# Kernel optimization log

Hardware: AMD Instinct MI355X
Metric: run time of the kernel (lower is better)

Reference implementation:

```python
import jax, jax.numpy as jnp
import numpy as np

N_LAGS = 64
EPS = 1e-8


def setup_inputs() -> dict:
    key = jax.random.key(0)
    x = jax.random.normal(key, (16, 8, 250, 1024), dtype=jnp.float32)
    return {"x": x}


def reference(x):
    B, M, T, L = x.shape
    # rfft over all mics once (shared across pairs)
    X = jnp.fft.rfft(x, axis=-1)  # [B, M, T, L//2+1] complex
    # all mic pairs (m1 < m2), row-major order matching the torch double loop
    i1, i2 = np.triu_indices(M, k=1)
    X1 = X[:, i1]  # [B, P, T, F]
    X2 = X[:, i2]  # [B, P, T, F]
    R = X1 * jnp.conj(X2)
    R = R / (jnp.abs(R) + EPS)  # PHAT weighting
    cc = jnp.fft.irfft(R, n=L, axis=-1)        # [B, P, T, L]
    cc = jnp.fft.fftshift(cc, axes=-1)
    center = L // 2
    start = center - N_LAGS // 2
    return cc[..., start:start + N_LAGS]        # [B, P, T, n_lags]
```

## Files before the change

kernel.cpp:

```cpp
#include <hip/hip_runtime.h>
#include <math.h>

#define B_    16
#define M_    8
#define T_    250
#define L_    1024
#define NPAIR 28

#define KTOT   1024
#define CH_K   128
#define NKT    4
#define NCHUNK 8

typedef _Float16 half8  __attribute__((ext_vector_type(8)));
typedef _Float16 half2t __attribute__((ext_vector_type(2)));
typedef float    floatx4 __attribute__((ext_vector_type(4)));

__device__ __align__(16) _Float16 g_Btw[64 * KTOT];

__constant__ int c_i1[NPAIR] = {0,0,0,0,0,0,0,1,1,1,1,1,1,2,2,2,2,2,3,3,3,3,4,4,4,5,5,6};
__constant__ int c_i2[NPAIR] = {1,2,3,4,5,6,7,2,3,4,5,6,7,3,4,5,6,7,4,5,6,7,5,6,7,6,7,7};

__global__ void init_btw() {
    int idx = blockIdx.x * 256 + threadIdx.x;
    int n = idx >> 10, k = idx & 1023;
    float v;
    if (k == 0)      v = 1.0f / 1024.0f;
    else if (k == 1) v = (n & 1) ? (-1.0f / 1024.0f) : (1.0f / 1024.0f);
    else {
        int bin = k >> 1, tau = n - 32;
        int r = (tau * bin) & 1023;
        float ang = (float)r * (6.283185307179586f / 1024.0f);
        float s, c; sincosf(ang, &s, &c);
        v = ((k & 1) ? -s : c) * (2.0f / 1024.0f);
    }
    g_Btw[idx] = (_Float16)v;
}

#define PHI(i) ((i) ^ (((i) >> 4) & 15) ^ ((((i) >> 8) & 3) << 1))
#define AXR(p) (8 * ((p) & 7))

__device__ inline float2 cmul(float2 a, float2 b) {
    return make_float2(fmaf(a.x, b.x, -a.y * b.y), fmaf(a.x, b.y, a.y * b.x));
}
__device__ inline float2 cadd(float2 a, float2 b) { return make_float2(a.x + b.x, a.y + b.y); }
__device__ inline float2 csub(float2 a, float2 b) { return make_float2(a.x - b.x, a.y - b.y); }
__device__ inline float2 cmni(float2 a) { return make_float2(a.y, -a.x); }

__device__ inline void dft8(float2 v[8]) {
    const float rt = 0.70710678118654752440f;
    float2 b0 = cadd(v[0], v[4]), b1 = cadd(v[1], v[5]);
    float2 b2 = cadd(v[2], v[6]), b3 = cadd(v[3], v[7]);
    float2 c0 = csub(v[0], v[4]);
    float2 t1 = csub(v[1], v[5]);
    float2 c1 = make_float2(rt * (t1.x + t1.y), rt * (t1.y - t1.x));
    float2 c2 = cmni(csub(v[2], v[6]));
    float2 t3 = csub(v[3], v[7]);
    float2 c3 = make_float2(rt * (t3.y - t3.x), -rt * (t3.x + t3.y));
    float2 f0 = cadd(b0, b2), f1 = cadd(b1, b3);
    float2 g0 = csub(b0, b2), g1 = cmni(csub(b1, b3));
    v[0] = cadd(f0, f1); v[4] = csub(f0, f1);
    v[2] = cadd(g0, g1); v[6] = csub(g0, g1);
    f0 = cadd(c0, c2); f1 = cadd(c1, c3);
    g0 = csub(c0, c2); g1 = cmni(csub(c1, c3));
    v[1] = cadd(f0, f1); v[5] = csub(f0, f1);
    v[3] = cadd(g0, g1); v[7] = csub(g0, g1);
}

__device__ inline void twiddle8(float2 v[8], float2 w1) {
    float2 w = w1;
    v[1] = cmul(v[1], w);
#pragma unroll
    for (int k = 2; k < 8; ++k) { w = cmul(w, w1); v[k] = cmul(v[k], w); }
}

__device__ inline int posmap(int k) {
    return ((k & 1) << 9) | (((k >> 1) & 7) << 6) | (((k >> 4) & 7) << 3) | ((k >> 7) & 7);
}

__global__ __launch_bounds__(512, 8) void gcc_main(const float* __restrict__ x,
                                                   float* __restrict__ out) {
    __shared__ float2 s_z[4 * 1024];
    __shared__ __align__(16) _Float16 sA[32 * CH_K];

    const int tid = threadIdx.x;
    const int t = blockIdx.x, b = blockIdx.y;
    const int f = tid & 127, c = tid >> 7;
    float2* Zb = s_z + c * 1024;

    float ws, wc;
    sincosf((float)f * (-6.283185307179586f / 1024.0f), &ws, &wc);
    const float2 w = make_float2(wc, ws);

    {
        const float* xa = x + (((size_t)b * M_ + 2 * c) * T_ + t) * L_;
        const float* xb = xa + (size_t)T_ * L_;
        float va[8], vb[8];
#pragma unroll
        for (int j = 0; j < 8; ++j) { va[j] = xa[f + 128 * j]; vb[j] = xb[f + 128 * j]; }
        const float rt = 0.70710678118654752440f;
#pragma unroll
        for (int q = 0; q < 4; ++q) {
            float2 a = make_float2(va[q], vb[q]);
            float2 d = make_float2(va[q + 4], vb[q + 4]);
            float2 tq = cmul(csub(a, d), w);
            float2 r;
            if (q == 0)      r = tq;
            else if (q == 1) r = make_float2(rt * (tq.x + tq.y), rt * (tq.y - tq.x));
            else if (q == 2) r = make_float2(tq.y, -tq.x);
            else             r = make_float2(rt * (tq.y - tq.x), -rt * (tq.x + tq.y));
            Zb[PHI(f + 128 * q)]       = cadd(a, d);
            Zb[PHI(f + 128 * q + 512)] = r;
        }
    }
    __syncthreads();

    {
        float2 wl = w;
        if (f & 64) wl = cmul(wl, make_float2(0.92387953251128674f, 0.38268343236508977f));
        const float2 wB = cmul(wl, wl);
        const int base = (f >> 6) * 512 + (f & 63);
        float2 v[8];
#pragma unroll
        for (int r = 0; r < 8; ++r) v[r] = Zb[PHI(base + 64 * r)];
        dft8(v);
        twiddle8(v, wB);
#pragma unroll
        for (int k = 0; k < 8; ++k) Zb[PHI(base + 64 * k)] = v[k];
    }
    __syncthreads();

    {
        float s2, c2;
        sincosf((float)(f & 7) * (-6.283185307179586f / 64.0f), &s2, &c2);
        const float2 wC = make_float2(c2, s2);
        const int base = (f >> 3) * 64 + (f & 7);
        float2 v[8];
#pragma unroll
        for (int r = 0; r < 8; ++r) v[r] = Zb[PHI(base + 8 * r)];
        dft8(v);
        twiddle8(v, wC);
#pragma unroll
        for (int k = 0; k < 8; ++k) Zb[PHI(base + 8 * k)] = v[k];
    }
    __syncthreads();

    {
        const int base = f * 8;
        float2 v[8];
#pragma unroll
        for (int r = 0; r < 8; ++r) v[r] = Zb[PHI(base + r)];
        dft8(v);
#pragma unroll
        for (int k = 0; k < 8; ++k) Zb[PHI(base + k)] = v[k];
    }
    __syncthreads();

    const int lane = tid & 63, wv = tid >> 6;
    const int mt = wv >> 2, nt = wv & 3;
    const int l15 = lane & 15, quad = lane >> 4;
    const int arow = mt * 16 + l15;
    const _Float16* Bbase = g_Btw + (nt * 16 + l15) * KTOT;
    floatx4 acc = {0.0f, 0.0f, 0.0f, 0.0f};

    const int bl = lane;
    const int pg = wv;

    if (tid < 256) ((unsigned int*)sA)[1792 + tid] = 0u;

#define PAIRA(p_, a_, b_)                                                     \
    {                                                                         \
        float2 X1 = Xs[a_], X2 = Xs[b_];                                      \
        float rr = X1.x * X2.x + X1.y * X2.y;                                 \
        float ri = X1.y * X2.x - X1.x * X2.y;                                 \
        float m2 = rr * rr + ri * ri;                                         \
        float inv = (m2 > 1e-30f) ? rsqrtf(m2) : 0.0f;                        \
        *(half2t*)&sA[(p_) * CH_K + ((2 * bl) ^ AXR(p_))] =                   \
            (half2t){(_Float16)(rr * inv), (_Float16)(ri * inv)};             \
    }

    auto fillA = [&](int h) {
        const int beta = h * 64 + bl;
        const int pa = posmap(beta);
        const int pb = posmap((1024 - beta) & 1023);
        float2 Xs[8];
#pragma unroll
        for (int cc = 0; cc < 4; ++cc) {
            float2 Aa = s_z[cc * 1024 + PHI(pa)];
            float2 Bb = s_z[cc * 1024 + PHI(pb)];
            Xs[2 * cc]     = make_float2(0.5f * (Aa.x + Bb.x), 0.5f * (Aa.y - Bb.y));
            Xs[2 * cc + 1] = make_float2(0.5f * (Aa.y + Bb.y), 0.5f * (Bb.x - Aa.x));
        }
        if (pg == 0) {
            PAIRA(0, 0, 1) PAIRA(1, 0, 2) PAIRA(2, 0, 3) PAIRA(3, 0, 4)
        } else if (pg == 1) {
            PAIRA(4, 0, 5) PAIRA(5, 0, 6) PAIRA(6, 0, 7) PAIRA(7, 1, 2)
        } else if (pg == 2) {
            PAIRA(8, 1, 3) PAIRA(9, 1, 4) PAIRA(10, 1, 5) PAIRA(11, 1, 6)
        } else if (pg == 3) {
            PAIRA(12, 1, 7) PAIRA(13, 2, 3) PAIRA(14, 2, 4) PAIRA(15, 2, 5)
        } else if (pg == 4) {
            PAIRA(16, 2, 6) PAIRA(17, 2, 7) PAIRA(18, 3, 4)
        } else if (pg == 5) {
            PAIRA(19, 3, 5) PAIRA(20, 3, 6) PAIRA(21, 3, 7)
        } else if (pg == 6) {
            PAIRA(22, 4, 5) PAIRA(23, 4, 6) PAIRA(24, 4, 7)
        } else {
            PAIRA(25, 5, 6) PAIRA(26, 5, 7) PAIRA(27, 6, 7)
        }
        if (h == 0 && bl == 0) {
            const int p0 = (pg < 4) ? 4 * pg : 16 + 3 * (pg - 4);
            const int cnt = (pg < 4) ? 4 : 3;
            const int pN = 4;
#pragma unroll
            for (int pp = 0; pp < cnt; ++pp) {
                const int p = p0 + pp;
                float2 Za = s_z[(c_i1[p] >> 1) * 1024 + pN];
                float2 Zc = s_z[(c_i2[p] >> 1) * 1024 + pN];
                float x1 = (c_i1[p] & 1) ? Za.y : Za.x;
                float x2 = (c_i2[p] & 1) ? Zc.y : Zc.x;
                float rr = x1 * x2;
                float inv = (rr * rr > 1e-30f) ? rsqrtf(rr * rr) : 0.0f;
                sA[p * CH_K + (1 ^ AXR(p))] = (_Float16)(rr * inv);
            }
        }
    };

    for (int h = 0; h < NCHUNK; ++h) {
        fillA(h);
        __syncthreads();

        const _Float16* Bp = Bbase + h * CH_K;
        const int ax = AXR(arow);
#pragma unroll
        for (int kt = 0; kt < NKT; ++kt) {
            half8 af = *(const half8*)(sA + arow * CH_K + ((kt * 32 + quad * 8) ^ ax));
            half8 bf = *(const half8*)(Bp + kt * 32 + quad * 8);
            acc = __builtin_amdgcn_mfma_f32_16x16x32_f16(af, bf, acc, 0, 0, 0);
        }
        __syncthreads();
    }

#pragma unroll
    for (int r = 0; r < 4; ++r) {
        int pair = mt * 16 + quad * 4 + r;
        if (pair < NPAIR)
            out[((((size_t)b * NPAIR + pair) * T_ + t) << 6) + nt * 16 + l15] = acc[r];
    }
}

extern "C" void kernel_launch(void* const* d_in, const int* in_sizes, int n_in,
                              void* d_out, int out_size, void* d_ws, size_t ws_size,
                              hipStream_t stream) {
    (void)in_sizes; (void)n_in; (void)d_ws; (void)ws_size; (void)out_size;
    hipLaunchKernelGGL(init_btw, dim3(256), dim3(256), 0, stream);
    hipLaunchKernelGGL(gcc_main, dim3(T_, B_), dim3(512), 0, stream,
                       (const float*)d_in[0], (float*)d_out);
}
```

Baseline: 320.6 us.

## Split fused FFT+PHAT+DFT kernel into FFT kernel and separate MFMA matmul kernel

The single fused kernel is split in two. The first does the per-frame FFT and PHAT weighting and writes the normalized cross-spectra as fp16 to a large global buffer. The second is a dedicated MFMA kernel where each wave computes all 28 pairs by 64 lags for one frame over the full K=1024, with more accumulators per wave. This removes per-chunk shared-memory staging and barriers from the matmul, but adds a write and read of a roughly 229 MB intermediate and one more kernel launch.

```diff
diff --git a/kernel.cpp b/kernel.cpp
--- a/kernel.cpp
+++ b/kernel.cpp
@@ -6,17 +6,14 @@
 #define T_    250
 #define L_    1024
 #define NPAIR 28
-
-#define KTOT   1024
-#define CH_K   128
-#define NKT    4
-#define NCHUNK 8
+#define NBT   (B_ * T_)
 
 typedef _Float16 half8  __attribute__((ext_vector_type(8)));
 typedef _Float16 half2t __attribute__((ext_vector_type(2)));
 typedef float    floatx4 __attribute__((ext_vector_type(4)));
 
-__device__ __align__(16) _Float16 g_Btw[64 * KTOT];
+__device__ __align__(16) _Float16 g_Btw[64 * 1024];
+__device__ __align__(16) _Float16 g_A[((size_t)NBT * NPAIR + 64) * 1024];
 
 __constant__ int c_i1[NPAIR] = {0,0,0,0,0,0,0,1,1,1,1,1,1,2,2,2,2,2,3,3,3,3,4,4,4,5,5,6};
 __constant__ int c_i2[NPAIR] = {1,2,3,4,5,6,7,2,3,4,5,6,7,3,4,5,6,7,4,5,6,7,5,6,7,6,7,7};
@@ -38,7 +35,6 @@
 }
 
 #define PHI(i) ((i) ^ (((i) >> 4) & 15) ^ ((((i) >> 8) & 3) << 1))
-#define AXR(p) (8 * ((p) & 7))
 
 __device__ inline float2 cmul(float2 a, float2 b) {
     return make_float2(fmaf(a.x, b.x, -a.y * b.y), fmaf(a.x, b.y, a.y * b.x));
@@ -78,10 +74,8 @@
     return ((k & 1) << 9) | (((k >> 1) & 7) << 6) | (((k >> 4) & 7) << 3) | ((k >> 7) & 7);
 }
 
-__global__ __launch_bounds__(512, 8) void gcc_main(const float* __restrict__ x,
-                                                   float* __restrict__ out) {
+__global__ __launch_bounds__(512, 6) void gcc_fft(const float* __restrict__ x) {
     __shared__ float2 s_z[4 * 1024];
-    __shared__ __align__(16) _Float16 sA[32 * CH_K];
 
     const int tid = threadIdx.x;
     const int t = blockIdx.x, b = blockIdx.y;
@@ -156,31 +150,23 @@
     }
     __syncthreads();
 
-    const int lane = tid & 63, wv = tid >> 6;
-    const int mt = wv >> 2, nt = wv & 3;
-    const int l15 = lane & 15, quad = lane >> 4;
-    const int arow = mt * 16 + l15;
-    const _Float16* Bbase = g_Btw + (nt * 16 + l15) * KTOT;
-    floatx4 acc = {0.0f, 0.0f, 0.0f, 0.0f};
-
-    const int bl = lane;
-    const int pg = wv;
-
-    if (tid < 256) ((unsigned int*)sA)[1792 + tid] = 0u;
-
-#define PAIRA(p_, a_, b_)                                                     \
+    const int bl = tid & 127, pg = tid >> 7;
+    const size_t abase = ((size_t)b * T_ + t) * (size_t)(NPAIR * 1024);
+
+#define PAIRG(p_, a_, b_)                                                     \
     {                                                                         \
         float2 X1 = Xs[a_], X2 = Xs[b_];                                      \
         float rr = X1.x * X2.x + X1.y * X2.y;                                 \
         float ri = X1.y * X2.x - X1.x * X2.y;                                 \
         float m2 = rr * rr + ri * ri;                                         \
         float inv = (m2 > 1e-30f) ? rsqrtf(m2) : 0.0f;                        \
-        *(half2t*)&sA[(p_) * CH_K + ((2 * bl) ^ AXR(p_))] =                   \
+        *(half2t*)&g_A[abase + (p_) * 1024 + 2 * beta] =                      \
             (half2t){(_Float16)(rr * inv), (_Float16)(ri * inv)};             \
     }
 
-    auto fillA = [&](int h) {
-        const int beta = h * 64 + bl;
+#pragma unroll 1
+    for (int h = 0; h < 4; ++h) {
+        const int beta = h * 128 + bl;
         const int pa = posmap(beta);
         const int pb = posmap((1024 - beta) & 1023);
         float2 Xs[8];
@@ -192,60 +178,81 @@
             Xs[2 * cc + 1] = make_float2(0.5f * (Aa.y + Bb.y), 0.5f * (Bb.x - Aa.x));
         }
         if (pg == 0) {
-            PAIRA(0, 0, 1) PAIRA(1, 0, 2) PAIRA(2, 0, 3) PAIRA(3, 0, 4)
+            PAIRG(0, 0, 1) PAIRG(1, 0, 2) PAIRG(2, 0, 3) PAIRG(3, 0, 4)
+            PAIRG(4, 0, 5) PAIRG(5, 0, 6) PAIRG(6, 0, 7)
         } else if (pg == 1) {
-            PAIRA(4, 0, 5) PAIRA(5, 0, 6) PAIRA(6, 0, 7) PAIRA(7, 1, 2)
+            PAIRG(7, 1, 2) PAIRG(8, 1, 3) PAIRG(9, 1, 4) PAIRG(10, 1, 5)
+            PAIRG(11, 1, 6) PAIRG(12, 1, 7) PAIRG(13, 2, 3)
         } else if (pg == 2) {
-            PAIRA(8, 1, 3) PAIRA(9, 1, 4) PAIRA(10, 1, 5) PAIRA(11, 1, 6)
-        } else if (pg == 3) {
-            PAIRA(12, 1, 7) PAIRA(13, 2, 3) PAIRA(14, 2, 4) PAIRA(15, 2, 5)
-        } else if (pg == 4) {
-            PAIRA(16, 2, 6) PAIRA(17, 2, 7) PAIRA(18, 3, 4)
-        } else if (pg == 5) {
-            PAIRA(19, 3, 5) PAIRA(20, 3, 6) PAIRA(21, 3, 7)
-        } else if (pg == 6) {
-            PAIRA(22, 4, 5) PAIRA(23, 4, 6) PAIRA(24, 4, 7)
+            PAIRG(14, 2, 4) PAIRG(15, 2, 5) PAIRG(16, 2, 6) PAIRG(17, 2, 7)
+            PAIRG(18, 3, 4) PAIRG(19, 3, 5) PAIRG(20, 3, 6)
         } else {
-            PAIRA(25, 5, 6) PAIRA(26, 5, 7) PAIRA(27, 6, 7)
+            PAIRG(21, 3, 7) PAIRG(22, 4, 5) PAIRG(23, 4, 6) PAIRG(24, 4, 7)
+            PAIRG(25, 5, 6) PAIRG(26, 5, 7) PAIRG(27, 6, 7)
         }
         if (h == 0 && bl == 0) {
-            const int p0 = (pg < 4) ? 4 * pg : 16 + 3 * (pg - 4);
-            const int cnt = (pg < 4) ? 4 : 3;
             const int pN = 4;
 #pragma unroll
-            for (int pp = 0; pp < cnt; ++pp) {
-                const int p = p0 + pp;
+            for (int pp = 0; pp < 7; ++pp) {
+                const int p = pg * 7 + pp;
                 float2 Za = s_z[(c_i1[p] >> 1) * 1024 + pN];
                 float2 Zc = s_z[(c_i2[p] >> 1) * 1024 + pN];
                 float x1 = (c_i1[p] & 1) ? Za.y : Za.x;
                 float x2 = (c_i2[p] & 1) ? Zc.y : Zc.x;
                 float rr = x1 * x2;
                 float inv = (rr * rr > 1e-30f) ? rsqrtf(rr * rr) : 0.0f;
-                sA[p * CH_K + (1 ^ AXR(p))] = (_Float16)(rr * inv);
+                g_A[abase + p * 1024 + 1] = (_Float16)(rr * inv);
             }
         }
-    };
-
-    for (int h = 0; h < NCHUNK; ++h) {
-        fillA(h);
-        __syncthreads();
-
-        const _Float16* Bp = Bbase + h * CH_K;
-        const int ax = AXR(arow);
-#pragma unroll
-        for (int kt = 0; kt < NKT; ++kt) {
-            half8 af = *(const half8*)(sA + arow * CH_K + ((kt * 32 + quad * 8) ^ ax));
-            half8 bf = *(const half8*)(Bp + kt * 32 + quad * 8);
-            acc = __builtin_amdgcn_mfma_f32_16x16x32_f16(af, bf, acc, 0, 0, 0);
-        }
-        __syncthreads();
-    }
-
+    }
+}
+
+__global__ __launch_bounds__(256, 4) void gcc_mm(float* __restrict__ out) {
+    const int lane = threadIdx.x & 63, wv = threadIdx.x >> 6;
+    const int bt = blockIdx.x * 4 + wv;
+    const int l15 = lane & 15, quad = lane >> 4;
+    const int b = bt / T_, t = bt - b * T_;
+
+    const _Float16* Ap0 = g_A + ((size_t)bt * NPAIR + l15) * 1024 + quad * 8;
+    const _Float16* Ap1 = Ap0 + 16 * 1024;
+    const _Float16* Bp  = g_Btw + (size_t)l15 * 1024 + quad * 8;
+
+    floatx4 acc00 = {0,0,0,0}, acc01 = {0,0,0,0}, acc02 = {0,0,0,0}, acc03 = {0,0,0,0};
+    floatx4 acc10 = {0,0,0,0}, acc11 = {0,0,0,0}, acc12 = {0,0,0,0}, acc13 = {0,0,0,0};
+
+#pragma unroll 4
+    for (int kt = 0; kt < 32; ++kt) {
+        half8 a0 = *(const half8*)(Ap0 + kt * 32);
+        half8 a1 = *(const half8*)(Ap1 + kt * 32);
+        half8 b0 = *(const half8*)(Bp + 0 * 16384 + kt * 32);
+        half8 b1 = *(const half8*)(Bp + 1 * 16384 + kt * 32);
+        half8 b2 = *(const half8*)(Bp + 2 * 16384 + kt * 32);
+        half8 b3 = *(const half8*)(Bp + 3 * 16384 + kt * 32);
+        acc00 = __builtin_amdgcn_mfma_f32_16x16x32_f16(a0, b0, acc00, 0, 0, 0);
+        acc10 = __builtin_amdgcn_mfma_f32_16x16x32_f16(a1, b0, acc10, 0, 0, 0);
+        acc01 = __builtin_amdgcn_mfma_f32_16x16x32_f16(a0, b1, acc01, 0, 0, 0);
+        acc11 = __builtin_amdgcn_mfma_f32_16x16x32_f16(a1, b1, acc11, 0, 0, 0);
+        acc02 = __builtin_amdgcn_mfma_f32_16x16x32_f16(a0, b2, acc02, 0, 0, 0);
+        acc12 = __builtin_amdgcn_mfma_f32_16x16x32_f16(a1, b2, acc12, 0, 0, 0);
+        acc03 = __builtin_amdgcn_mfma_f32_16x16x32_f16(a0, b3, acc03, 0, 0, 0);
+        acc13 = __builtin_amdgcn_mfma_f32_16x16x32_f16(a1, b3, acc13, 0, 0, 0);
+    }
+
+    const size_t obase = (((size_t)b * NPAIR) * T_ + t) << 6;
 #pragma unroll
     for (int r = 0; r < 4; ++r) {
-        int pair = mt * 16 + quad * 4 + r;
-        if (pair < NPAIR)
-            out[((((size_t)b * NPAIR + pair) * T_ + t) << 6) + nt * 16 + l15] = acc[r];
+        int p0 = quad * 4 + r;
+        out[obase + ((size_t)p0 * T_ << 6) + 0 * 16 + l15] = acc00[r];
+        out[obase + ((size_t)p0 * T_ << 6) + 1 * 16 + l15] = acc01[r];
+        out[obase + ((size_t)p0 * T_ << 6) + 2 * 16 + l15] = acc02[r];
+        out[obase + ((size_t)p0 * T_ << 6) + 3 * 16 + l15] = acc03[r];
+        int p1 = 16 + quad * 4 + r;
+        if (p1 < NPAIR) {
+            out[obase + ((size_t)p1 * T_ << 6) + 0 * 16 + l15] = acc10[r];
+            out[obase + ((size_t)p1 * T_ << 6) + 1 * 16 + l15] = acc11[r];
+            out[obase + ((size_t)p1 * T_ << 6) + 2 * 16 + l15] = acc12[r];
+            out[obase + ((size_t)p1 * T_ << 6) + 3 * 16 + l15] = acc13[r];
+        }
     }
 }
 
@@ -254,6 +261,6 @@
                               hipStream_t stream) {
     (void)in_sizes; (void)n_in; (void)d_ws; (void)ws_size; (void)out_size;
     hipLaunchKernelGGL(init_btw, dim3(256), dim3(256), 0, stream);
-    hipLaunchKernelGGL(gcc_main, dim3(T_, B_), dim3(512), 0, stream,
-                       (const float*)d_in[0], (float*)d_out);
-}
+    hipLaunchKernelGGL(gcc_fft, dim3(T_, B_), dim3(512), 0, stream, (const float*)d_in[0]);
+    hipLaunchKernelGGL(gcc_mm, dim3(NBT / 4), dim3(256), 0, stream, (float*)d_out);
+}
```

Measured after the change: 362.3 us. +13.0%, slower.

## Double-buffer PHAT A tiles and prefetch twiddle B fragments into registers

Applied to the files above, without the earlier changes.

The A operand in shared memory is now double-buffered, so the next chunk's PHAT-normalised cross-spectrum is written while MFMAs consume the current one. This removes one barrier per chunk. The twiddle-matrix B fragments for the next chunk are loaded into registers one iteration ahead. The XOR swizzle is replaced by a padded row pitch of 136, and the launch-bounds occupancy hint drops from 8 to 4. The cost is more LDS per block and more registers, which may lower occupancy. Rows 28-31 of the A buffers are no longer zeroed, which relies on those MFMA output rows never being written.

```diff
diff --git a/kernel.cpp b/kernel.cpp
--- a/kernel.cpp
+++ b/kernel.cpp
@@ -7,16 +7,17 @@
 #define L_    1024
 #define NPAIR 28
 
-#define KTOT   1024
 #define CH_K   128
 #define NKT    4
 #define NCHUNK 8
+#define APITCH 136
+#define ABUF   (32 * APITCH)
 
 typedef _Float16 half8  __attribute__((ext_vector_type(8)));
 typedef _Float16 half2t __attribute__((ext_vector_type(2)));
 typedef float    floatx4 __attribute__((ext_vector_type(4)));
 
-__device__ __align__(16) _Float16 g_Btw[64 * KTOT];
+__device__ __align__(16) _Float16 g_Btw[64 * 1024];
 
 __constant__ int c_i1[NPAIR] = {0,0,0,0,0,0,0,1,1,1,1,1,1,2,2,2,2,2,3,3,3,3,4,4,4,5,5,6};
 __constant__ int c_i2[NPAIR] = {1,2,3,4,5,6,7,2,3,4,5,6,7,3,4,5,6,7,4,5,6,7,5,6,7,6,7,7};
@@ -38,7 +39,6 @@
 }
 
 #define PHI(i) ((i) ^ (((i) >> 4) & 15) ^ ((((i) >> 8) & 3) << 1))
-#define AXR(p) (8 * ((p) & 7))
 
 __device__ inline float2 cmul(float2 a, float2 b) {
     return make_float2(fmaf(a.x, b.x, -a.y * b.y), fmaf(a.x, b.y, a.y * b.x));
@@ -78,10 +78,10 @@
     return ((k & 1) << 9) | (((k >> 1) & 7) << 6) | (((k >> 4) & 7) << 3) | ((k >> 7) & 7);
 }
 
-__global__ __launch_bounds__(512, 8) void gcc_main(const float* __restrict__ x,
+__global__ __launch_bounds__(512, 4) void gcc_main(const float* __restrict__ x,
                                                    float* __restrict__ out) {
     __shared__ float2 s_z[4 * 1024];
-    __shared__ __align__(16) _Float16 sA[32 * CH_K];
+    __shared__ __align__(16) _Float16 sA[2 * ABUF];
 
     const int tid = threadIdx.x;
     const int t = blockIdx.x, b = blockIdx.y;
@@ -160,13 +160,11 @@
     const int mt = wv >> 2, nt = wv & 3;
     const int l15 = lane & 15, quad = lane >> 4;
     const int arow = mt * 16 + l15;
-    const _Float16* Bbase = g_Btw + (nt * 16 + l15) * KTOT;
+    const _Float16* Bbase = g_Btw + (size_t)(nt * 16 + l15) * 1024 + quad * 8;
     floatx4 acc = {0.0f, 0.0f, 0.0f, 0.0f};
 
     const int bl = lane;
     const int pg = wv;
-
-    if (tid < 256) ((unsigned int*)sA)[1792 + tid] = 0u;
 
 #define PAIRA(p_, a_, b_)                                                     \
     {                                                                         \
@@ -175,11 +173,11 @@
         float ri = X1.y * X2.x - X1.x * X2.y;                                 \
         float m2 = rr * rr + ri * ri;                                         \
         float inv = (m2 > 1e-30f) ? rsqrtf(m2) : 0.0f;                        \
-        *(half2t*)&sA[(p_) * CH_K + ((2 * bl) ^ AXR(p_))] =                   \
+        *(half2t*)&dst[(p_) * APITCH + 2 * bl] =                              \
             (half2t){(_Float16)(rr * inv), (_Float16)(ri * inv)};             \
     }
 
-    auto fillA = [&](int h) {
+    auto fillA = [&](int h, _Float16* dst) {
         const int beta = h * 64 + bl;
         const int pa = posmap(beta);
         const int pb = posmap((1024 - beta) & 1023);
@@ -221,24 +219,35 @@
                 float x2 = (c_i2[p] & 1) ? Zc.y : Zc.x;
                 float rr = x1 * x2;
                 float inv = (rr * rr > 1e-30f) ? rsqrtf(rr * rr) : 0.0f;
-                sA[p * CH_K + (1 ^ AXR(p))] = (_Float16)(rr * inv);
+                dst[p * APITCH + 1] = (_Float16)(rr * inv);
             }
         }
     };
 
+    half8 bc[4], bn[4];
+#pragma unroll
+    for (int kt = 0; kt < NKT; ++kt) bc[kt] = *(const half8*)(Bbase + kt * 32);
+
+    fillA(0, sA);
+    __syncthreads();
+
+#pragma unroll
     for (int h = 0; h < NCHUNK; ++h) {
-        fillA(h);
-        __syncthreads();
-
-        const _Float16* Bp = Bbase + h * CH_K;
-        const int ax = AXR(arow);
+        if (h < NCHUNK - 1) {
+            const _Float16* Bn = Bbase + (h + 1) * CH_K;
+#pragma unroll
+            for (int kt = 0; kt < NKT; ++kt) bn[kt] = *(const half8*)(Bn + kt * 32);
+            fillA(h + 1, sA + ((h + 1) & 1) * ABUF);
+        }
+        const _Float16* Ap = sA + (h & 1) * ABUF + arow * APITCH;
 #pragma unroll
         for (int kt = 0; kt < NKT; ++kt) {
-            half8 af = *(const half8*)(sA + arow * CH_K + ((kt * 32 + quad * 8) ^ ax));
-            half8 bf = *(const half8*)(Bp + kt * 32 + quad * 8);
-            acc = __builtin_amdgcn_mfma_f32_16x16x32_f16(af, bf, acc, 0, 0, 0);
-        }
-        __syncthreads();
+            half8 af = *(const half8*)(Ap + kt * 32 + quad * 8);
+            acc = __builtin_amdgcn_mfma_f32_16x16x32_f16(af, bc[kt], acc, 0, 0, 0);
+        }
+#pragma unroll
+        for (int kt = 0; kt < NKT; ++kt) bc[kt] = bn[kt];
+        if (h < NCHUNK - 1) __syncthreads();
     }
 
 #pragma unroll
```

Result: slower. 373.2 us (+16.4%).

## Double GEMM K-chunk, use padded sA pitch, and rebalance pair-fill work

Applied to the files above, without the earlier changes.

The PHAT-weighted A tile now covers 256 frequency columns instead of 128. That halves the fill/MFMA rounds and the block-wide barriers. The XOR swizzle on sA is replaced by a padded row pitch of 264. Pair normalization is redistributed so each 128-thread group handles 7 pairs. The twiddle powers are computed as a shallower tree rather than a serial chain, and launch bounds drop to 4 blocks/SM to match the larger LDS footprint. The zero-fill of the unused A rows is removed; those rows only feed outputs that are never written.

```diff
diff --git a/kernel.cpp b/kernel.cpp
--- a/kernel.cpp
+++ b/kernel.cpp
@@ -8,9 +8,10 @@
 #define NPAIR 28
 
 #define KTOT   1024
-#define CH_K   128
-#define NKT    4
-#define NCHUNK 8
+#define CH_K   256
+#define NKT    8
+#define NCHUNK 4
+#define APITCH 264
 
 typedef _Float16 half8  __attribute__((ext_vector_type(8)));
 typedef _Float16 half2t __attribute__((ext_vector_type(2)));
@@ -38,7 +39,6 @@
 }
 
 #define PHI(i) ((i) ^ (((i) >> 4) & 15) ^ ((((i) >> 8) & 3) << 1))
-#define AXR(p) (8 * ((p) & 7))
 
 __device__ inline float2 cmul(float2 a, float2 b) {
     return make_float2(fmaf(a.x, b.x, -a.y * b.y), fmaf(a.x, b.y, a.y * b.x));
@@ -68,20 +68,25 @@
 }
 
 __device__ inline void twiddle8(float2 v[8], float2 w1) {
-    float2 w = w1;
-    v[1] = cmul(v[1], w);
-#pragma unroll
-    for (int k = 2; k < 8; ++k) { w = cmul(w, w1); v[k] = cmul(v[k], w); }
+    float2 w2 = cmul(w1, w1);
+    float2 w3 = cmul(w2, w1);
+    float2 w4 = cmul(w2, w2);
+    float2 w5 = cmul(w4, w1);
+    float2 w6 = cmul(w4, w2);
+    float2 w7 = cmul(w4, w3);
+    v[1] = cmul(v[1], w1); v[2] = cmul(v[2], w2); v[3] = cmul(v[3], w3);
+    v[4] = cmul(v[4], w4); v[5] = cmul(v[5], w5); v[6] = cmul(v[6], w6);
+    v[7] = cmul(v[7], w7);
 }
 
 __device__ inline int posmap(int k) {
     return ((k & 1) << 9) | (((k >> 1) & 7) << 6) | (((k >> 4) & 7) << 3) | ((k >> 7) & 7);
 }
 
-__global__ __launch_bounds__(512, 8) void gcc_main(const float* __restrict__ x,
+__global__ __launch_bounds__(512, 4) void gcc_main(const float* __restrict__ x,
                                                    float* __restrict__ out) {
     __shared__ float2 s_z[4 * 1024];
-    __shared__ __align__(16) _Float16 sA[32 * CH_K];
+    __shared__ __align__(16) _Float16 sA[32 * APITCH];
 
     const int tid = threadIdx.x;
     const int t = blockIdx.x, b = blockIdx.y;
@@ -163,10 +168,7 @@
     const _Float16* Bbase = g_Btw + (nt * 16 + l15) * KTOT;
     floatx4 acc = {0.0f, 0.0f, 0.0f, 0.0f};
 
-    const int bl = lane;
-    const int pg = wv;
-
-    if (tid < 256) ((unsigned int*)sA)[1792 + tid] = 0u;
+    const int bl = tid & 127, pg = tid >> 7;
 
 #define PAIRA(p_, a_, b_)                                                     \
     {                                                                         \
@@ -175,12 +177,12 @@
         float ri = X1.y * X2.x - X1.x * X2.y;                                 \
         float m2 = rr * rr + ri * ri;                                         \
         float inv = (m2 > 1e-30f) ? rsqrtf(m2) : 0.0f;                        \
-        *(half2t*)&sA[(p_) * CH_K + ((2 * bl) ^ AXR(p_))] =                   \
+        *(half2t*)&sA[(p_) * APITCH + 2 * bl] =                               \
             (half2t){(_Float16)(rr * inv), (_Float16)(ri * inv)};             \
     }
 
     auto fillA = [&](int h) {
-        const int beta = h * 64 + bl;
+        const int beta = h * 128 + bl;
         const int pa = posmap(beta);
         const int pb = posmap((1024 - beta) & 1023);
         float2 Xs[8];
@@ -193,35 +195,29 @@
         }
         if (pg == 0) {
             PAIRA(0, 0, 1) PAIRA(1, 0, 2) PAIRA(2, 0, 3) PAIRA(3, 0, 4)
+            PAIRA(4, 0, 5) PAIRA(5, 0, 6) PAIRA(6, 0, 7)
         } else if (pg == 1) {
-            PAIRA(4, 0, 5) PAIRA(5, 0, 6) PAIRA(6, 0, 7) PAIRA(7, 1, 2)
+            PAIRA(7, 1, 2) PAIRA(8, 1, 3) PAIRA(9, 1, 4) PAIRA(10, 1, 5)
+            PAIRA(11, 1, 6) PAIRA(12, 1, 7) PAIRA(13, 2, 3)
         } else if (pg == 2) {
-            PAIRA(8, 1, 3) PAIRA(9, 1, 4) PAIRA(10, 1, 5) PAIRA(11, 1, 6)
-        } else if (pg == 3) {
-            PAIRA(12, 1, 7) PAIRA(13, 2, 3) PAIRA(14, 2, 4) PAIRA(15, 2, 5)
-        } else if (pg == 4) {
-            PAIRA(16, 2, 6) PAIRA(17, 2, 7) PAIRA(18, 3, 4)
-        } else if (pg == 5) {
-            PAIRA(19, 3, 5) PAIRA(20, 3, 6) PAIRA(21, 3, 7)
-        } else if (pg == 6) {
-            PAIRA(22, 4, 5) PAIRA(23, 4, 6) PAIRA(24, 4, 7)
+            PAIRA(14, 2, 4) PAIRA(15, 2, 5) PAIRA(16, 2, 6) PAIRA(17, 2, 7)
+            PAIRA(18, 3, 4) PAIRA(19, 3, 5) PAIRA(20, 3, 6)
         } else {
+            PAIRA(21, 3, 7) PAIRA(22, 4, 5) PAIRA(23, 4, 6) PAIRA(24, 4, 7)
             PAIRA(25, 5, 6) PAIRA(26, 5, 7) PAIRA(27, 6, 7)
         }
         if (h == 0 && bl == 0) {
-            const int p0 = (pg < 4) ? 4 * pg : 16 + 3 * (pg - 4);
-            const int cnt = (pg < 4) ? 4 : 3;
             const int pN = 4;
 #pragma unroll
-            for (int pp = 0; pp < cnt; ++pp) {
-                const int p = p0 + pp;
+            for (int pp = 0; pp < 7; ++pp) {
+                const int p = pg * 7 + pp;
                 float2 Za = s_z[(c_i1[p] >> 1) * 1024 + pN];
                 float2 Zc = s_z[(c_i2[p] >> 1) * 1024 + pN];
                 float x1 = (c_i1[p] & 1) ? Za.y : Za.x;
                 float x2 = (c_i2[p] & 1) ? Zc.y : Zc.x;
                 float rr = x1 * x2;
                 float inv = (rr * rr > 1e-30f) ? rsqrtf(rr * rr) : 0.0f;
-                sA[p * CH_K + (1 ^ AXR(p))] = (_Float16)(rr * inv);
+                sA[p * APITCH + 1] = (_Float16)(rr * inv);
             }
         }
     };
@@ -230,11 +226,11 @@
         fillA(h);
         __syncthreads();
 
+        const _Float16* Ap = sA + arow * APITCH;
         const _Float16* Bp = Bbase + h * CH_K;
-        const int ax = AXR(arow);
 #pragma unroll
         for (int kt = 0; kt < NKT; ++kt) {
-            half8 af = *(const half8*)(sA + arow * CH_K + ((kt * 32 + quad * 8) ^ ax));
+            half8 af = *(const half8*)(Ap + kt * 32 + quad * 8);
             half8 bf = *(const half8*)(Bp + kt * 32 + quad * 8);
             acc = __builtin_amdgcn_mfma_f32_16x16x32_f16(af, bf, acc, 0, 0, 0);
         }
```

Measured after the change: 296.6 us. 7.5% less time.
